# Performance work log

Hardware: AMD Instinct MI355X
Metric: run time of the kernel (lower is better)

Reference implementation:

```python
import jax, jax.numpy as jnp
import numpy as np

PATCH_NUMS = (1, 2, 3, 4, 5, 6, 8, 10, 13, 16)
MAX_PN = 16
N_PHI = 4
RESI_RATIO = 0.5
TOK_T = 1.0  # tokenize_temperature


def _area_matrix(n_in, n_out):
    # F.interpolate(mode='area') == adaptive_avg_pool: equal-weight fractional bins
    M = np.zeros((n_out, n_in), np.float32)
    for i in range(n_out):
        s = (i * n_in) // n_out
        e = -((-(i + 1) * n_in) // n_out)  # ceil
        M[i, s:e] = 1.0 / (e - s)
    return M


def _cubic(t, a=-0.75):
    t = abs(float(t))
    if t <= 1.0:
        return (a + 2) * t ** 3 - (a + 3) * t ** 2 + 1.0
    if t < 2.0:
        return a * t ** 3 - 5 * a * t ** 2 + 8 * a * t - 4 * a
    return 0.0


def _bicubic_matrix(n_in, n_out):
    # PyTorch bicubic, align_corners=False, a=-0.75, edge-clamped taps
    M = np.zeros((n_out, n_in), np.float32)
    scale = n_in / n_out
    for j in range(n_out):
        src = (j + 0.5) * scale - 0.5
        fi = int(np.floor(src))
        t = src - fi
        for k in range(-1, 3):
            idx = min(max(fi + k, 0), n_in - 1)
            M[j, idx] += _cubic(k - t)
    return M


def _resize_sep(x, M):
    # separable spatial resize: x [B,C,H,W] -> [B,C,out,out]
    y = jnp.einsum('ph,bchw->bcpw', M, x)
    return jnp.einsum('qw,bcpw->bcpq', M, y)


def setup_inputs() -> dict:
    key = jax.random.key(0)
    k1, k2, k3 = jax.random.split(key, 3)
    feat = jax.random.normal(k1, (128, 32, 16, 16), jnp.float32)
    codebook = jax.random.normal(k2, (4096, 32), jnp.float32)
    phi_w = jax.random.normal(k3, (N_PHI, 32, 32, 3, 3), jnp.float32) * 0.05
    phi_b = jnp.zeros((N_PHI, 32), jnp.float32)
    return {"feat": feat, "codebook": codebook, "phi_w": phi_w, "phi_b": phi_b}


def reference(feat, codebook, phi_w, phi_b):
    B, C, H, W = feat.shape
    K = len(PATCH_NUMS)
    denom = max(K - 1, 1)
    c2 = jnp.sum(codebook * codebook, axis=-1)  # [V]
    f_rest = feat
    f_hat = jnp.zeros_like(feat)
    contexts = []
    for si, pn in enumerate(PATCH_NUMS):
        if si < K - 1:
            A = jnp.asarray(_area_matrix(H, pn))
            z = _resize_sep(f_rest, A)
        else:
            z = f_rest
        zt = z.transpose(0, 2, 3, 1).reshape(B, pn * pn, C)  # [B, pn^2, C]
        x2 = jnp.sum(zt * zt, axis=-1, keepdims=True)
        logits = -(x2 + c2[None, None, :] - 2.0 * jnp.einsum('bnc,vc->bnv', zt, codebook))
        probs = jax.nn.softmax(logits / max(TOK_T, 1e-6), axis=-1)
        idx = jnp.argmax(probs, axis=-1)
        hard = codebook[idx]                                   # [B, pn^2, C]
        soft = jnp.einsum('bnv,vc->bnc', probs, codebook)
        emb = hard + soft - jax.lax.stop_gradient(soft)        # STE (fwd value == hard)
        h = emb.reshape(B, pn, pn, C).transpose(0, 3, 1, 2)    # [B, C, pn, pn]
        if si < K - 1:
            U = jnp.asarray(_bicubic_matrix(pn, MAX_PN))
            h_up = _resize_sep(h, U)
        else:
            h_up = h
        pi = int(round(si / denom * (N_PHI - 1)))              # quant_resi[si/denom]
        conv = jax.lax.conv_general_dilated(
            h_up, phi_w[pi], (1, 1), 'SAME',
            dimension_numbers=('NCHW', 'OIHW', 'NCHW')) + phi_b[pi][None, :, None, None]
        h_up = h_up * (1.0 - RESI_RATIO) + conv * RESI_RATIO
        f_hat = f_hat + h_up
        f_rest = f_rest - h_up
        if pn < MAX_PN:
            fk = _resize_sep(f_hat, jnp.asarray(_area_matrix(H, pn)))
        else:
            fk = f_hat
        contexts.append(fk.reshape(B, C, pn * pn).transpose(0, 2, 1))  # [B, pn^2, C]
    return jnp.concatenate(contexts, axis=1)  # [B, 680, C]
```

## Files before the change

### kernel.cpp

```cpp
#include <hip/hip_runtime.h>

#define B 128
#define C 32
#define HH 16
#define V 4096
#define MARGIN 1e-4f

typedef __attribute__((ext_vector_type(8))) short bf16x8;
typedef __attribute__((ext_vector_type(4))) float f32x4;


__device__ __forceinline__ float cubicw(float t) {
    float at = fabsf(t);
    float at2 = at * at, at3 = at2 * at;
    if (at <= 1.f) return 1.25f * at3 - 2.25f * at2 + 1.f;
    if (at < 2.f)  return -0.75f * at3 + 3.75f * at2 - 6.f * at + 3.f;
    return 0.f;
}

__device__ __forceinline__ unsigned short f2bf_rne(float f) {
    unsigned int u = __float_as_uint(f);
    unsigned int r = (u + 0x7fffu + ((u >> 16) & 1u)) >> 16;
    return (unsigned short)r;
}
__device__ __forceinline__ float bf2f(unsigned short h) {
    return __uint_as_float(((unsigned int)h) << 16);
}


__global__ void setup_kernel(const float* __restrict__ feat, float* __restrict__ f_rest,
                             float* __restrict__ f_hat, const float* __restrict__ cb,
                             double* __restrict__ c2d, float* __restrict__ c2f,
                             float* __restrict__ z0, unsigned short* __restrict__ cbh,
                             unsigned short* __restrict__ cbl) {
    int i = blockIdx.x * 256 + threadIdx.x;
    if (i < B * C * HH * HH) { f_rest[i] = feat[i]; f_hat[i] = 0.f; }
    if (i < V) {
        const float* p = cb + i * C;
        double s = 0.0;
        #pragma unroll
        for (int j = 0; j < C; ++j) { double d = (double)p[j]; s = fma(d, d, s); }
        c2d[i] = s;
        c2f[i] = (float)s;
    }
    if (i < B * C) {
        const float* p = feat + i * (HH * HH);
        float s = 0.f;
        for (int px = 0; px < HH * HH; ++px) s += p[px];
        z0[i] = s * (1.f / 256.f);
    }
    if (i < V * C) {
        int ii = i & 7, nn = (i >> 3) & 15, kb = (i >> 7) & 3, T = i >> 9;
        float val = cb[(T * 16 + nn) * C + kb * 8 + ii];
        unsigned short h = f2bf_rne(val);
        cbh[i] = h;
        cbl[i] = f2bf_rne(val - bf2f(h));
    }
}

__global__ __launch_bounds__(256, 4) void scan_mfma_kernel(
    const float* __restrict__ z, const unsigned short* __restrict__ cbh,
    const unsigned short* __restrict__ cbl, const float* __restrict__ c2f,
    float4* __restrict__ pk, int npx, int nseg, int ngrp)
{
    int tid = threadIdx.x;
    int wave = tid >> 6, lane = tid & 63;
    int job = blockIdx.x * 4 + wave;
    int seg = job / ngrp, tokgrp = job - seg * ngrp;
    int cps = V / nseg;
    int total = B * npx;
    int tn = lane & 15, kb = lane >> 4;

    __shared__ alignas(16) char ldsu[26112];
    short* ldsA = (short*)ldsu;
    float* smb1 = (float*)ldsu;
    float* smb2 = (float*)(ldsu + 8704);
    int*   smi1 = (int*)(ldsu + 17408);

    {
        #pragma unroll
        for (int g = 0; g < 2; ++g) {
            int tok = tokgrp * 32 + g * 16 + tn;
            int bq = tok / npx, n = tok - bq * npx;
            short hi[8], lo[8];
            #pragma unroll
            for (int i = 0; i < 8; ++i) {
                float v = z[(bq * C + kb * 8 + i) * npx + n];
                unsigned short h = f2bf_rne(v);
                hi[i] = (short)h;
                lo[i] = (short)f2bf_rne(v - bf2f(h));
            }
            short* sh_ = ldsA + ((wave * 4 + g * 2) * 64 + lane) * 8;
            short* sl_ = ldsA + ((wave * 4 + g * 2 + 1) * 64 + lane) * 8;
            #pragma unroll
            for (int i = 0; i < 8; ++i) { sh_[i] = hi[i]; sl_[i] = lo[i]; }
        }
    }
    __syncthreads();

    const bf16x8* fp = reinterpret_cast<const bf16x8*>(ldsA);
    const bf16x8* ph = reinterpret_cast<const bf16x8*>(cbh);
    const bf16x8* pl = reinterpret_cast<const bf16x8*>(cbl);

    float b1[8], b2[8]; int i1[8];
    #pragma unroll
    for (int s = 0; s < 8; ++s) { b1[s] = 3e38f; b2[s] = 3e38f; i1[s] = 0; }

    int T0 = seg * (cps >> 4), nT = cps >> 4;
    bf16x8 bh = ph[(size_t)T0 * 64 + lane];
    bf16x8 bl = pl[(size_t)T0 * 64 + lane];
    float c2v = c2f[T0 * 16 + tn];

    #pragma unroll 1
    for (int t = 0; t < nT; ++t) {
        asm volatile("" ::: "memory");
        bf16x8 a0h = fp[(wave * 4 + 0) * 64 + lane];
        bf16x8 a0l = fp[(wave * 4 + 1) * 64 + lane];
        bf16x8 a1h = fp[(wave * 4 + 2) * 64 + lane];
        bf16x8 a1l = fp[(wave * 4 + 3) * 64 + lane];

        int Tn = T0 + ((t + 1 < nT) ? t + 1 : t);
        bf16x8 nbh = ph[(size_t)Tn * 64 + lane];
        bf16x8 nbl = pl[(size_t)Tn * 64 + lane];
        float nc2 = c2f[Tn * 16 + tn];

        f32x4 a0 = {0.f, 0.f, 0.f, 0.f}, a1 = {0.f, 0.f, 0.f, 0.f};
        a0 = __builtin_amdgcn_mfma_f32_16x16x32_bf16(a0h, bh, a0, 0, 0, 0);
        a0 = __builtin_amdgcn_mfma_f32_16x16x32_bf16(a0l, bh, a0, 0, 0, 0);
        a0 = __builtin_amdgcn_mfma_f32_16x16x32_bf16(a0h, bl, a0, 0, 0, 0);
        a0 = __builtin_amdgcn_mfma_f32_16x16x32_bf16(a0l, bl, a0, 0, 0, 0);
        a1 = __builtin_amdgcn_mfma_f32_16x16x32_bf16(a1h, bh, a1, 0, 0, 0);
        a1 = __builtin_amdgcn_mfma_f32_16x16x32_bf16(a1l, bh, a1, 0, 0, 0);
        a1 = __builtin_amdgcn_mfma_f32_16x16x32_bf16(a1h, bl, a1, 0, 0, 0);
        a1 = __builtin_amdgcn_mfma_f32_16x16x32_bf16(a1l, bl, a1, 0, 0, 0);

        int code = (T0 + t) * 16 + tn;
        #pragma unroll
        for (int r = 0; r < 4; ++r) {
            float s0 = fmaf(-2.f, a0[r], c2v);
            if (s0 < b1[r]) { b2[r] = b1[r]; b1[r] = s0; i1[r] = code; }
            else if (s0 < b2[r]) { b2[r] = s0; }
            float s1 = fmaf(-2.f, a1[r], c2v);
            if (s1 < b1[4 + r]) { b2[4 + r] = b1[4 + r]; b1[4 + r] = s1; i1[4 + r] = code; }
            else if (s1 < b2[4 + r]) { b2[4 + r] = s1; }
        }
        bh = nbh; bl = nbl; c2v = nc2;
    }

    __syncthreads();
    #pragma unroll
    for (int g = 0; g < 2; ++g)
        #pragma unroll
        for (int r = 0; r < 4; ++r) {
            int tokl = g * 16 + kb * 4 + r;
            int base = wave * 544 + tokl * 17 + tn;
            smb1[base] = b1[g * 4 + r];
            smb2[base] = b2[g * 4 + r];
            smi1[base] = i1[g * 4 + r];
        }
    __syncthreads();
    if (tid < 128) {
        int w = tid >> 5, tl = tid & 31;
        int jobw = blockIdx.x * 4 + w;
        int segw = jobw / ngrp, tgw = jobw - segw * ngrp;
        float gb1 = 3e38f, gb2 = 3e38f; int gi1 = 0;
        #pragma unroll
        for (int i = 0; i < 16; ++i) {
            float v1 = smb1[w * 544 + tl * 17 + i];
            int   ix = smi1[w * 544 + tl * 17 + i];
            if (v1 < gb1 || (v1 == gb1 && ix < gi1)) { gb2 = gb1; gb1 = v1; gi1 = ix; }
            else if (v1 < gb2) { gb2 = v1; }
            float v2 = smb2[w * 544 + tl * 17 + i];
            if (v2 < gb2) gb2 = v2;
        }
        int tok = tgw * 32 + tl;
        float4 o;
        o.x = gb1; o.y = gb2; o.z = __int_as_float(gi1); o.w = 0.f;
        pk[(size_t)segw * total + tok] = o;
    }
}

__global__ __launch_bounds__(256) void stage_tail_kernel(
    const float4* __restrict__ pk, const float* __restrict__ z,
    const float* __restrict__ cb, const double* __restrict__ c2d,
    const float* __restrict__ w, const float* __restrict__ bias,
    float* __restrict__ f_hat, float* __restrict__ f_rest,
    float* __restrict__ out, float* __restrict__ znext,
    int pn, int off, int pn2, int nseg)
{
    int bb = blockIdx.x >> 2;
    int og = (blockIdx.x & 3) * 8;
    int tid = threadIdx.x;
    int npx = pn * pn;
    int total = B * npx;

    __shared__ float A_s[32][257];
    __shared__ float Bc[16][257];
    __shared__ alignas(16) float w_s[8 * 384];
    __shared__ int idx_s[256];
    __shared__ int flist[256];
    __shared__ int fcnt;
    __shared__ double zsd[C];
    __shared__ double sred[256];
    __shared__ int sidx[256];
    __shared__ float wtab[16][4];
    __shared__ int   itab[16][4];
    float (*fh_s)[257] = &A_s[0];
    float (*fr_s)[257] = &A_s[8];

    float pf[8], pr[8];
    #pragma unroll
    for (int o = 0; o < 8; ++o) {
        int gi = (bb * 32 + og + o) * 256 + tid;
        pf[o] = f_hat[gi]; pr[o] = f_rest[gi];
    }
    for (int e = tid; e < 8 * 288; e += 256) {
        int o = e / 288, r = e - o * 288;
        w_s[o * 384 + (r / 9) * 12 + (r % 9)] = w[(size_t)og * 288 + e];
    }

    if (tid < 16) {
        float scale = (float)pn * (1.f / 16.f);
        float src = (tid + 0.5f) * scale - 0.5f;
        int fi = (int)floorf(src);
        float t = src - (float)fi;
        #pragma unroll
        for (int k = 0; k < 4; ++k) {
            wtab[tid][k] = cubicw((float)(k - 1) - t);
            itab[tid][k] = min(max(fi + k - 1, 0), pn - 1);
        }
    }
    if (tid == 0) fcnt = 0;
    __syncthreads();

    if (tid < npx) {
        int tok = bb * npx + tid;
        float gb1 = 3e38f, gb2 = 3e38f; int gi1 = 0;
        for (int s = 0; s < nseg; ++s) {
            float4 e = pk[(size_t)s * total + tok];
            float v1 = e.x; int ix = __float_as_int(e.z);
            if (v1 < gb1 || (v1 == gb1 && ix < gi1)) { gb2 = gb1; gb1 = v1; gi1 = ix; }
            else if (v1 < gb2) { gb2 = v1; }
            if (e.y < gb2) gb2 = e.y;
        }
        idx_s[tid] = gi1;
        if (gb2 - gb1 < MARGIN) { int slot = atomicAdd(&fcnt, 1); flist[slot] = tid; }
    }
    __syncthreads();

    int nf = fcnt;
    for (int f = 0; f < nf; ++f) {
        int n = flist[f];
        if (tid < C) zsd[tid] = (double)z[(bb * C + tid) * npx + n];
        __syncthreads();
        double best = 1e300; int bi = 0x7fffffff;
        for (int k = 0; k < V / 256; ++k) {
            int v = tid + k * 256;
            const float4* cp = reinterpret_cast<const float4*>(cb + (size_t)v * C);
            double acc = 0.0;
            #pragma unroll
            for (int qq = 0; qq < 8; ++qq) {
                float4 fv = cp[qq];
                acc = fma((double)fv.x, zsd[4 * qq + 0], acc);
                acc = fma((double)fv.y, zsd[4 * qq + 1], acc);
                acc = fma((double)fv.z, zsd[4 * qq + 2], acc);
                acc = fma((double)fv.w, zsd[4 * qq + 3], acc);
            }
            double s = fma(-2.0, acc, c2d[v]);
            if (s < best || (s == best && v < bi)) { best = s; bi = v; }
        }
        sred[tid] = best; sidx[tid] = bi;
        __syncthreads();
        for (int st = 128; st > 0; st >>= 1) {
            if (tid < st) {
                double o = sred[tid + st]; int oi = sidx[tid + st];
                double me = sred[tid];     int mi = sidx[tid];
                if (o < me || (o == me && oi < mi)) { sred[tid] = o; sidx[tid] = oi; }
            }
            __syncthreads();
        }
        if (tid == 0) idx_s[n] = sidx[0];
        __syncthreads();
    }
    __syncthreads();

    for (int e = tid; e < 32 * npx; e += 256) {
        int c = e & 31, n = e >> 5;
        A_s[c][n] = cb[idx_s[n] * 32 + c];
    }
    __syncthreads();

    #pragma unroll 1
    for (int ch = 0; ch < 2; ++ch) {
        for (int e = tid; e < 16 * 16 * pn; e += 256) {
            int wx = e % pn; int rest = e / pn;
            int p = rest & 15, cl = rest >> 4;
            float s = 0.f;
            #pragma unroll
            for (int k = 0; k < 4; ++k)
                s = fmaf(wtab[p][k], A_s[ch * 16 + cl][itab[p][k] * pn + wx], s);
            Bc[cl][p * pn + wx] = s;
        }
        __syncthreads();
        #pragma unroll
        for (int it = 0; it < 16; ++it) {
            int e = tid + it * 256;
            int q = e & 15, p = (e >> 4) & 15, cl = e >> 8;
            float s = 0.f;
            #pragma unroll
            for (int k = 0; k < 4; ++k)
                s = fmaf(wtab[q][k], Bc[cl][p * pn + itab[q][k]], s);
            A_s[ch * 16 + cl][e & 255] = s;
        }
        __syncthreads();
    }

    int p = tid >> 4, q = tid & 15;
    float acc[8];
    #pragma unroll
    for (int o = 0; o < 8; ++o) acc[o] = bias[og + o];
    for (int i = 0; i < 32; ++i) {
        float v[9];
        #pragma unroll
        for (int dy = 0; dy < 3; ++dy)
            #pragma unroll
            for (int dx = 0; dx < 3; ++dx) {
                int pp = p + dy - 1, qq = q + dx - 1;
                bool in = (pp >= 0) & (pp < 16) & (qq >= 0) & (qq < 16);
                v[dy * 3 + dx] = in ? A_s[i][pp * 16 + qq] : 0.f;
            }
        #pragma unroll
        for (int o = 0; o < 8; ++o) {
            const float* wr = &w_s[o * 384 + i * 12];
            float4 wa = *reinterpret_cast<const float4*>(wr);
            float4 wb = *reinterpret_cast<const float4*>(wr + 4);
            float w8 = wr[8];
            acc[o] = fmaf(wa.x, v[0], acc[o]); acc[o] = fmaf(wa.y, v[1], acc[o]);
            acc[o] = fmaf(wa.z, v[2], acc[o]); acc[o] = fmaf(wa.w, v[3], acc[o]);
            acc[o] = fmaf(wb.x, v[4], acc[o]); acc[o] = fmaf(wb.y, v[5], acc[o]);
            acc[o] = fmaf(wb.z, v[6], acc[o]); acc[o] = fmaf(wb.w, v[7], acc[o]);
            acc[o] = fmaf(w8,   v[8], acc[o]);
        }
    }
    float hv[8];
    #pragma unroll
    for (int o = 0; o < 8; ++o) hv[o] = A_s[og + o][tid];
    __syncthreads();

    #pragma unroll
    for (int o = 0; o < 8; ++o) {
        int gi = (bb * 32 + og + o) * 256 + tid;
        float blend = 0.5f * hv[o] + 0.5f * acc[o];
        float nf2 = pf[o] + blend;
        float nr2 = pr[o] - blend;
        f_hat[gi] = nf2; f_rest[gi] = nr2;
        fh_s[o][tid] = nf2; fr_s[o][tid] = nr2;
    }
    __syncthreads();

    for (int e = tid; e < 8 * npx; e += 256) {
        int o = e & 7, n = e >> 3;
        int y = n / pn, x = n - y * pn;
        int sh = (y * HH) / pn, eh = ((y + 1) * HH + pn - 1) / pn;
        int sw = (x * HH) / pn, ew = ((x + 1) * HH + pn - 1) / pn;
        float s = 0.f;
        for (int yy = sh; yy < eh; ++yy)
            for (int xx = sw; xx < ew; ++xx) s += fh_s[o][yy * 16 + xx];
        out[((bb * 680) + off + n) * 32 + og + o] = s * (1.f / (float)((eh - sh) * (ew - sw)));
    }

    if (pn2 > 0) {
        int npx2 = pn2 * pn2;
        for (int e = tid; e < 8 * npx2; e += 256) {
            int o = e / npx2, n = e - o * npx2;
            int y = n / pn2, x = n - y * pn2;
            int sh = (y * HH) / pn2, eh = ((y + 1) * HH + pn2 - 1) / pn2;
            int sw = (x * HH) / pn2, ew = ((x + 1) * HH + pn2 - 1) / pn2;
            float s = 0.f;
            for (int yy = sh; yy < eh; ++yy)
                for (int xx = sw; xx < ew; ++xx) s += fr_s[o][yy * 16 + xx];
            znext[(bb * 32 + og + o) * npx2 + n] = s * (1.f / (float)((eh - sh) * (ew - sw)));
        }
    }
}


extern "C" void kernel_launch(void* const* d_in, const int* in_sizes, int n_in,
                              void* d_out, int out_size, void* d_ws, size_t ws_size,
                              hipStream_t stream) {
    const float* feat = (const float*)d_in[0];
    const float* cb   = (const float*)d_in[1];
    const float* phiw = (const float*)d_in[2];
    const float* phib = (const float*)d_in[3];
    float* out = (float*)d_out;
    float* wsf = (float*)d_ws;

    const int NE = B * C * HH * HH;
    float* f_rest = wsf;
    float* f_hat  = wsf + NE;
    float* zA     = wsf + 2 * NE;
    float* zB     = wsf + 3 * NE;
    char*  tl     = (char*)(wsf + 4 * NE);
    double* c2d  = (double*)tl;
    float*  c2f  = (float*)(tl + (32 << 10));
    float4* pk   = (float4*)(tl + (48 << 10));
    unsigned short* cbh = (unsigned short*)(tl + (48 << 10) + (4 << 20));
    unsigned short* cbl = (unsigned short*)(tl + (48 << 10) + (4 << 20) + (512 << 10));

    static const int PN_[10]   = {1, 2, 3, 4, 5, 6, 8, 10, 13, 16};
    static const int PI_[10]   = {0, 0, 1, 1, 1, 2, 2, 2, 3, 3};
    static const int OFF_[10]  = {0, 1, 5, 14, 30, 55, 91, 155, 255, 424};
    static const int NSEG_[10] = {32, 32, 32, 16, 16, 16, 8, 8, 8, 8};

    setup_kernel<<<dim3((NE + 255) / 256), dim3(256), 0, stream>>>(
        feat, f_rest, f_hat, cb, c2d, c2f, zA, cbh, cbl);

    for (int si = 0; si < 10; ++si) {
        int pn = PN_[si], npx = pn * pn;
        int tokens = B * npx;
        int nseg = NSEG_[si];
        int ngrp = tokens / 32;
        int njobs = ngrp * nseg;
        float* zin  = (si & 1) ? zB : zA;
        float* zout = (si & 1) ? zA : zB;

        scan_mfma_kernel<<<dim3(njobs / 4), dim3(256), 0, stream>>>(
            zin, cbh, cbl, c2f, pk, npx, nseg, ngrp);

        int pn2 = (si < 9) ? PN_[si + 1] : 0;
        stage_tail_kernel<<<dim3(B * 4), dim3(256), 0, stream>>>(
            pk, zin, cb, c2d,
            phiw + PI_[si] * C * C * 9, phib + PI_[si] * C,
            f_hat, f_rest, out, zout, pn, OFF_[si], pn2, nseg);
    }
}
```

Baseline: 835.2 us.

## Shrink scan tile to 16 tokens per wave with register-resident A operands

The codebook-scan kernel now processes 16 tokens per wave instead of 32. The split-bf16 A fragments stay in registers rather than being staged in LDS, and the software prefetch of the next codebook tile is removed. The launch-bounds occupancy hint is dropped and the grid doubles (ngrp = tokens/16) to raise parallelism. In exchange, each codebook tile fetched from memory is reused across half as many tokens, so codebook load traffic per token doubles and global load latency is no longer hidden by prefetch.

```diff
diff --git a/kernel.cpp b/kernel.cpp
--- a/kernel.cpp
+++ b/kernel.cpp
@@ -58,7 +58,7 @@
     }
 }
 
-__global__ __launch_bounds__(256, 4) void scan_mfma_kernel(
+__global__ __launch_bounds__(256) void scan_mfma_kernel(
     const float* __restrict__ z, const unsigned short* __restrict__ cbh,
     const unsigned short* __restrict__ cbl, const float* __restrict__ c2f,
     float4* __restrict__ pk, int npx, int nseg, int ngrp)
@@ -71,109 +71,76 @@
     int total = B * npx;
     int tn = lane & 15, kb = lane >> 4;
 
-    __shared__ alignas(16) char ldsu[26112];
-    short* ldsA = (short*)ldsu;
-    float* smb1 = (float*)ldsu;
-    float* smb2 = (float*)(ldsu + 8704);
-    int*   smi1 = (int*)(ldsu + 17408);
-
+    __shared__ float smb1[4][16 * 17];
+    __shared__ float smb2[4][16 * 17];
+    __shared__ int   smi1[4][16 * 17];
+
+    bf16x8 ah, al;
     {
-        #pragma unroll
-        for (int g = 0; g < 2; ++g) {
-            int tok = tokgrp * 32 + g * 16 + tn;
-            int bq = tok / npx, n = tok - bq * npx;
-            short hi[8], lo[8];
-            #pragma unroll
-            for (int i = 0; i < 8; ++i) {
-                float v = z[(bq * C + kb * 8 + i) * npx + n];
-                unsigned short h = f2bf_rne(v);
-                hi[i] = (short)h;
-                lo[i] = (short)f2bf_rne(v - bf2f(h));
-            }
-            short* sh_ = ldsA + ((wave * 4 + g * 2) * 64 + lane) * 8;
-            short* sl_ = ldsA + ((wave * 4 + g * 2 + 1) * 64 + lane) * 8;
-            #pragma unroll
-            for (int i = 0; i < 8; ++i) { sh_[i] = hi[i]; sl_[i] = lo[i]; }
-        }
-    }
-    __syncthreads();
-
-    const bf16x8* fp = reinterpret_cast<const bf16x8*>(ldsA);
+        int tok = tokgrp * 16 + tn;
+        int bq = tok / npx, n = tok - bq * npx;
+        #pragma unroll
+        for (int i = 0; i < 8; ++i) {
+            float v = z[(bq * C + kb * 8 + i) * npx + n];
+            unsigned short h = f2bf_rne(v);
+            ah[i] = (short)h;
+            al[i] = (short)f2bf_rne(v - bf2f(h));
+        }
+    }
+
     const bf16x8* ph = reinterpret_cast<const bf16x8*>(cbh);
     const bf16x8* pl = reinterpret_cast<const bf16x8*>(cbl);
 
-    float b1[8], b2[8]; int i1[8];
-    #pragma unroll
-    for (int s = 0; s < 8; ++s) { b1[s] = 3e38f; b2[s] = 3e38f; i1[s] = 0; }
+    float b1[4], b2[4]; int i1[4];
+    #pragma unroll
+    for (int s = 0; s < 4; ++s) { b1[s] = 3e38f; b2[s] = 3e38f; i1[s] = 0; }
 
     int T0 = seg * (cps >> 4), nT = cps >> 4;
-    bf16x8 bh = ph[(size_t)T0 * 64 + lane];
-    bf16x8 bl = pl[(size_t)T0 * 64 + lane];
-    float c2v = c2f[T0 * 16 + tn];
-
     #pragma unroll 1
     for (int t = 0; t < nT; ++t) {
-        asm volatile("" ::: "memory");
-        bf16x8 a0h = fp[(wave * 4 + 0) * 64 + lane];
-        bf16x8 a0l = fp[(wave * 4 + 1) * 64 + lane];
-        bf16x8 a1h = fp[(wave * 4 + 2) * 64 + lane];
-        bf16x8 a1l = fp[(wave * 4 + 3) * 64 + lane];
-
-        int Tn = T0 + ((t + 1 < nT) ? t + 1 : t);
-        bf16x8 nbh = ph[(size_t)Tn * 64 + lane];
-        bf16x8 nbl = pl[(size_t)Tn * 64 + lane];
-        float nc2 = c2f[Tn * 16 + tn];
-
-        f32x4 a0 = {0.f, 0.f, 0.f, 0.f}, a1 = {0.f, 0.f, 0.f, 0.f};
-        a0 = __builtin_amdgcn_mfma_f32_16x16x32_bf16(a0h, bh, a0, 0, 0, 0);
-        a0 = __builtin_amdgcn_mfma_f32_16x16x32_bf16(a0l, bh, a0, 0, 0, 0);
-        a0 = __builtin_amdgcn_mfma_f32_16x16x32_bf16(a0h, bl, a0, 0, 0, 0);
-        a0 = __builtin_amdgcn_mfma_f32_16x16x32_bf16(a0l, bl, a0, 0, 0, 0);
-        a1 = __builtin_amdgcn_mfma_f32_16x16x32_bf16(a1h, bh, a1, 0, 0, 0);
-        a1 = __builtin_amdgcn_mfma_f32_16x16x32_bf16(a1l, bh, a1, 0, 0, 0);
-        a1 = __builtin_amdgcn_mfma_f32_16x16x32_bf16(a1h, bl, a1, 0, 0, 0);
-        a1 = __builtin_amdgcn_mfma_f32_16x16x32_bf16(a1l, bl, a1, 0, 0, 0);
-
-        int code = (T0 + t) * 16 + tn;
+        int T = T0 + t;
+        bf16x8 bh = ph[(size_t)T * 64 + lane];
+        bf16x8 bl = pl[(size_t)T * 64 + lane];
+        float c2v = c2f[T * 16 + tn];
+
+        f32x4 a0 = {0.f, 0.f, 0.f, 0.f};
+        a0 = __builtin_amdgcn_mfma_f32_16x16x32_bf16(ah, bh, a0, 0, 0, 0);
+        a0 = __builtin_amdgcn_mfma_f32_16x16x32_bf16(al, bh, a0, 0, 0, 0);
+        a0 = __builtin_amdgcn_mfma_f32_16x16x32_bf16(ah, bl, a0, 0, 0, 0);
+        a0 = __builtin_amdgcn_mfma_f32_16x16x32_bf16(al, bl, a0, 0, 0, 0);
+
+        int code = T * 16 + tn;
         #pragma unroll
         for (int r = 0; r < 4; ++r) {
             float s0 = fmaf(-2.f, a0[r], c2v);
             if (s0 < b1[r]) { b2[r] = b1[r]; b1[r] = s0; i1[r] = code; }
             else if (s0 < b2[r]) { b2[r] = s0; }
-            float s1 = fmaf(-2.f, a1[r], c2v);
-            if (s1 < b1[4 + r]) { b2[4 + r] = b1[4 + r]; b1[4 + r] = s1; i1[4 + r] = code; }
-            else if (s1 < b2[4 + r]) { b2[4 + r] = s1; }
-        }
-        bh = nbh; bl = nbl; c2v = nc2;
-    }
-
-    __syncthreads();
-    #pragma unroll
-    for (int g = 0; g < 2; ++g)
-        #pragma unroll
-        for (int r = 0; r < 4; ++r) {
-            int tokl = g * 16 + kb * 4 + r;
-            int base = wave * 544 + tokl * 17 + tn;
-            smb1[base] = b1[g * 4 + r];
-            smb2[base] = b2[g * 4 + r];
-            smi1[base] = i1[g * 4 + r];
-        }
-    __syncthreads();
-    if (tid < 128) {
-        int w = tid >> 5, tl = tid & 31;
+        }
+    }
+
+    #pragma unroll
+    for (int r = 0; r < 4; ++r) {
+        int tokl = kb * 4 + r;
+        smb1[wave][tokl * 17 + tn] = b1[r];
+        smb2[wave][tokl * 17 + tn] = b2[r];
+        smi1[wave][tokl * 17 + tn] = i1[r];
+    }
+    __syncthreads();
+    if (tid < 64) {
+        int w = tid >> 4, tl = tid & 15;
         int jobw = blockIdx.x * 4 + w;
         int segw = jobw / ngrp, tgw = jobw - segw * ngrp;
         float gb1 = 3e38f, gb2 = 3e38f; int gi1 = 0;
         #pragma unroll
         for (int i = 0; i < 16; ++i) {
-            float v1 = smb1[w * 544 + tl * 17 + i];
-            int   ix = smi1[w * 544 + tl * 17 + i];
+            float v1 = smb1[w][tl * 17 + i];
+            int   ix = smi1[w][tl * 17 + i];
             if (v1 < gb1 || (v1 == gb1 && ix < gi1)) { gb2 = gb1; gb1 = v1; gi1 = ix; }
             else if (v1 < gb2) { gb2 = v1; }
-            float v2 = smb2[w * 544 + tl * 17 + i];
+            float v2 = smb2[w][tl * 17 + i];
             if (v2 < gb2) gb2 = v2;
         }
-        int tok = tgw * 32 + tl;
+        int tok = tgw * 16 + tl;
         float4 o;
         o.x = gb1; o.y = gb2; o.z = __int_as_float(gi1); o.w = 0.f;
         pk[(size_t)segw * total + tok] = o;
@@ -419,7 +386,7 @@
         int pn = PN_[si], npx = pn * pn;
         int tokens = B * npx;
         int nseg = NSEG_[si];
-        int ngrp = tokens / 32;
+        int ngrp = tokens / 16;
         int njobs = ngrp * nseg;
         float* zin  = (si & 1) ? zB : zA;
         float* zout = (si & 1) ? zA : zB;
```

Measured after the change: 687.6 us. 17.7% less time.
